# Performance work log

Measured on AMD Instinct MI355X. Metric: run time of the kernel, lower is better.

Reference implementation:

```python
import jax, jax.numpy as jnp
import numpy as np

D_MODEL = 1024
NUM_HEADS = 16
D_K = D_MODEL // NUM_HEADS  # 64


def setup_inputs() -> dict:
    key = jax.random.key(0)
    k1, k2, k3, k4, k5 = jax.random.split(key, 5)
    scale = 1.0 / np.sqrt(D_MODEL)
    x = jax.random.normal(k1, (2, 8192, D_MODEL), dtype=jnp.float32)
    W_qkv = jax.random.normal(k2, (D_MODEL, 3 * D_MODEL), dtype=jnp.float32) * scale
    b_qkv = jax.random.normal(k3, (3 * D_MODEL,), dtype=jnp.float32) * 0.01
    W_out = jax.random.normal(k4, (D_MODEL, D_MODEL), dtype=jnp.float32) * scale
    b_out = jax.random.normal(k5, (D_MODEL,), dtype=jnp.float32) * 0.01
    return {"x": x, "W_qkv": W_qkv, "b_qkv": b_qkv, "W_out": W_out, "b_out": b_out}


def reference(x, W_qkv, b_qkv, W_out, b_out):
    B, S, _ = x.shape
    # qkv: [B, S, 3*d_model] -> reshape [B, S, H, 3*d_k] (matches torch reshape:
    # head h owns contiguous slice [h*3dk:(h+1)*3dk], split into q/k/v of d_k each)
    qkv = (jnp.einsum('bsd,de->bse', x, W_qkv) + b_qkv).reshape(B, S, NUM_HEADS, 3 * D_K)
    q, k, v = qkv[..., :D_K], qkv[..., D_K:2 * D_K], qkv[..., 2 * D_K:]
    # NOTE: faithful to source — no head transpose, so matmul contracts d_k and
    # produces scores across the HEAD axis: [B, S, H, H]
    scores = jnp.einsum('bshd,bsgd->bshg', q, k) / np.sqrt(D_K)
    attn = jax.nn.softmax(scores, axis=-1)  # softmax over heads (g)
    context = jnp.einsum('bshg,bsgd->bshd', attn, v).reshape(B, S, NUM_HEADS * D_K)
    return jnp.einsum('bsd,de->bse', context, W_out) + b_out
```

## Files before the change

### kernel.cpp

```cpp
#include <hip/hip_runtime.h>
#include <hip/hip_bf16.h>

typedef short bf16x8 __attribute__((ext_vector_type(8)));
typedef float f32x4 __attribute__((ext_vector_type(4)));
typedef ushort ushort8_t __attribute__((ext_vector_type(8)));

__device__ __forceinline__ float bf2f(ushort u) {
    union { unsigned int i; float f; } c; c.i = ((unsigned int)u) << 16; return c.f;
}
__device__ __forceinline__ ushort f2bf(float f) {
    union { float f; unsigned int i; } c; c.f = f;
    unsigned int x = c.i;
    return (ushort)((x + 0x7fffu + ((x >> 16) & 1u)) >> 16);
}

#define GLOAD_LDS16(g, l) __builtin_amdgcn_global_load_lds( \
    (const __attribute__((address_space(1))) unsigned int*)(g), \
    (__attribute__((address_space(3))) unsigned int*)(l), 16, 0, 0)

__device__ __forceinline__ void transpose_cvt_body(const float* __restrict__ in,
                                                   ushort* __restrict__ out,
                                                   int K, int N, int bx, int by,
                                                   int tid, float (*tile)[33]) {
    int n0 = bx * 32, k0 = by * 32;
    int tx = tid & 31, ty = tid >> 5;
    #pragma unroll
    for (int i = 0; i < 32; i += 8)
        tile[ty + i][tx] = in[(size_t)(k0 + ty + i) * N + n0 + tx];
    __syncthreads();
    #pragma unroll
    for (int i = 0; i < 32; i += 8)
        out[(size_t)(n0 + ty + i) * K + k0 + tx] = f2bf(tile[tx][ty + i]);
}

__global__ __launch_bounds__(256) void k_prep(const float* __restrict__ x,
                                              ushort* __restrict__ xb,
                                              const float* __restrict__ Wq,
                                              ushort* __restrict__ wqkT,
                                              const float* __restrict__ Wo,
                                              ushort* __restrict__ woT) {
    __shared__ float tile[32][33];
    const int b = blockIdx.x, tid = threadIdx.x;
    if (b < 16384) {
        int i = b * 256 + tid;
        float4 v = ((const float4*)x)[i];
        ushort4 o;
        o.x = f2bf(v.x); o.y = f2bf(v.y); o.z = f2bf(v.z); o.w = f2bf(v.w);
        ((ushort4*)xb)[i] = o;
    } else if (b < 16384 + 3072) {
        int idx = b - 16384;
        transpose_cvt_body(Wq, wqkT, 1024, 3072, idx % 96, idx / 96, tid, tile);
    } else {
        int idx = b - (16384 + 3072);
        transpose_cvt_body(Wo, woT, 1024, 1024, idx & 31, idx >> 5, tid, tile);
    }
}


#define LDSA(c,kk) (lds + (c)*65536 + (kk)*16384)
#define LDSB(c,kk) (lds + (c)*65536 + 32768 + (kk)*16384)
#define STAGE_A(c,kk,col) do { \
    GLOAD_LDS16(gA0 + (col), LDSA(c,kk) + wave*1024); \
    GLOAD_LDS16(gA1 + (col), LDSA(c,kk) + 8192 + wave*1024); } while(0)
#define STAGE_B(c,kk,col) do { \
    GLOAD_LDS16(gB0 + (col), LDSB(c,kk) + wave*1024); \
    GLOAD_LDS16(gB1 + (col), LDSB(c,kk) + 8192 + wave*1024); } while(0)
#define READ_A8(c,kk) do { const char* _p = LDSA(c,kk) + aoff; \
    _Pragma("unroll") for (int m = 0; m < 8; ++m) af[m] = *(const bf16x8*)(_p + m*1024); } while(0)
#define READ_B2(c,kk,n0) do { const char* _p = LDSB(c,kk) + boff; \
    bfr[n0] = *(const bf16x8*)(_p + (n0)*1024); \
    bfr[(n0)+1] = *(const bf16x8*)(_p + ((n0)+1)*1024); } while(0)
#define MF16(n0) do { __builtin_amdgcn_s_setprio(1); \
    _Pragma("unroll") for (int m = 0; m < 8; ++m) { \
    acc[m][n0]     = __builtin_amdgcn_mfma_f32_16x16x32_bf16(af[m], bfr[n0],     acc[m][n0],     0,0,0); \
    acc[m][(n0)+1] = __builtin_amdgcn_mfma_f32_16x16x32_bf16(af[m], bfr[(n0)+1], acc[m][(n0)+1], 0,0,0); } \
    __builtin_amdgcn_s_setprio(0); } while(0)

#define BAR __builtin_amdgcn_s_barrier()
#define SB0 __builtin_amdgcn_sched_barrier(0)
#define VM10 asm volatile("s_waitcnt vmcnt(10)")
#define VM0  asm volatile("s_waitcnt vmcnt(0)")

#define PH1(reads, stage, mf, vm) do { reads; stage; mf; SB0; vm; BAR; SB0; } while(0)

#define ITERX(kb, LAST) do { \
   PH1( { READ_A8(0,0); READ_B2(0,0,0); }, STAGE_B(1,1,(kb)+96),              MF16(0), ); \
   PH1( { READ_B2(0,0,2); },               if(!(LAST)) STAGE_A(0,0,(kb)+128), MF16(2), if(LAST) VM0; else VM10 ); \
   PH1( { READ_A8(0,1); READ_B2(0,1,0); }, if(!(LAST)) STAGE_B(0,0,(kb)+128), MF16(0), ); \
   PH1( { READ_B2(0,1,2); },               if(!(LAST)) STAGE_A(0,1,(kb)+160), MF16(2), if(!(LAST)) VM10 ); \
   PH1( { READ_A8(1,0); READ_B2(1,0,0); }, if(!(LAST)) STAGE_B(0,1,(kb)+160), MF16(0), ); \
   PH1( { READ_B2(1,0,2); },               if(!(LAST)) STAGE_A(1,0,(kb)+192), MF16(2), if(!(LAST)) VM10 ); \
   PH1( { READ_A8(1,1); READ_B2(1,1,0); }, if(!(LAST)) STAGE_B(1,0,(kb)+192), MF16(0), ); \
   PH1( { READ_B2(1,1,2); },               if(!(LAST)) STAGE_A(1,1,(kb)+224), MF16(2), if(!(LAST)) VM10 ); \
} while(0)

template<bool OUT_BF16>
__global__ __launch_bounds__(512, 2) void k_gemm256(const ushort* __restrict__ A,
                                                    const ushort* __restrict__ Bt,
                                                    const float* __restrict__ bias,
                                                    void* __restrict__ Cout,
                                                    int N, int NTN) {
    __shared__ __align__(16) char lds[131072];
    const int K = 1024;
    const int tid = threadIdx.x;
    const int wave = tid >> 6, lane = tid & 63;
    const int wr = wave >> 2, wc = wave & 3;
    const int r = lane & 15, q = lane >> 4;

    const int cpx = gridDim.x >> 3, wg = blockIdx.x;
    const int swz = (wg & 7) * cpx + (wg >> 3);
    const int tm = swz / NTN, tn = swz - tm * NTN;
    const int bm = tm * 256, bn = tn * 256;

    const int srow = tid >> 2;
    const int c16l = (tid & 3) ^ ((srow >> 1) & 3);
    const ushort* gA0 = A  + (size_t)(bm + srow) * K + c16l * 8;
    const ushort* gA1 = gA0 + (size_t)128 * K;
    const ushort* gB0 = Bt + (size_t)(bn + srow) * K + c16l * 8;
    const ushort* gB1 = gB0 + (size_t)128 * K;

    const int chunkx = ((q ^ ((r >> 1) & 3)) << 4);
    const int aoff = (wr * 128 + r) * 64 + chunkx;
    const int boff = (wc * 64 + r) * 64 + chunkx;

    f32x4 acc[8][4];
    #pragma unroll
    for (int m = 0; m < 8; ++m)
        #pragma unroll
        for (int n = 0; n < 4; ++n)
            acc[m][n] = (f32x4){0.f, 0.f, 0.f, 0.f};
    bf16x8 af[8], bfr[4];

    STAGE_A(0,0,0);  STAGE_B(0,0,0);
    STAGE_A(0,1,32); STAGE_B(0,1,32);
    STAGE_A(1,0,64); STAGE_B(1,0,64);
    STAGE_A(1,1,96);
    VM10; BAR; SB0;

    #pragma unroll 1
    for (int i = 0; i < 7; ++i) { ITERX(i * 128, 0); }
    ITERX(896, 1);

    float* Cf = (float*)Cout;
    ushort* Cb = (ushort*)Cout;
    #pragma unroll
    for (int m = 0; m < 8; ++m) {
        int row0 = bm + wr * 128 + m * 16 + q * 4;
        #pragma unroll
        for (int n = 0; n < 4; ++n) {
            int col = bn + wc * 64 + n * 16 + r;
            float bv = bias[col];
            #pragma unroll
            for (int j = 0; j < 4; ++j) {
                float v = acc[m][n][j] + bv;
                if (OUT_BF16) Cb[(size_t)(row0 + j) * N + col] = f2bf(v);
                else          Cf[(size_t)(row0 + j) * N + col] = v;
            }
        }
    }
}

__global__ __launch_bounds__(256) void k_attn_mfma(const ushort* __restrict__ qkv,
                                                   ushort* __restrict__ ctx) {
    const int lane = threadIdx.x & 63;
    const size_t tok = (size_t)blockIdx.x * 4 + (threadIdx.x >> 6);
    const ushort* row = qkv + tok * 3072;
    const int r = lane & 15, g = lane >> 4;

    bf16x8 ka[2], qb[2];
    #pragma unroll
    for (int c = 0; c < 2; ++c) {
        ka[c] = *(const bf16x8*)(row + r * 192 + 64 + c * 32 + g * 8);
        qb[c] = *(const bf16x8*)(row + r * 192 +      c * 32 + g * 8);
    }
    f32x4 st = (f32x4){0.f, 0.f, 0.f, 0.f};
    st = __builtin_amdgcn_mfma_f32_16x16x32_bf16(ka[0], qb[0], st, 0, 0, 0);
    st = __builtin_amdgcn_mfma_f32_16x16x32_bf16(ka[1], qb[1], st, 0, 0, 0);

    float s[4];
    #pragma unroll
    for (int j = 0; j < 4; ++j) s[j] = st[j] * 0.125f;
    float m = fmaxf(fmaxf(s[0], s[1]), fmaxf(s[2], s[3]));
    m = fmaxf(m, __shfl_xor(m, 16));
    m = fmaxf(m, __shfl_xor(m, 32));
    float p[4], sum = 0.f;
    #pragma unroll
    for (int j = 0; j < 4; ++j) { p[j] = __expf(s[j] - m); sum += p[j]; }
    sum += __shfl_xor(sum, 16);
    sum += __shfl_xor(sum, 32);
    float inv = 1.f / sum;
    #pragma unroll
    for (int j = 0; j < 4; ++j) p[j] *= inv;

    const bool gok = (g < 2);
    const int src0 = (r + 32 * g) & 63, src1 = (src0 + 16) & 63;
    bf16x8 pa;
    #pragma unroll
    for (int j = 0; j < 4; ++j) {
        float a0 = __shfl(p[j], src0, 64);
        float a1 = __shfl(p[j], src1, 64);
        pa[j]     = (short)(gok ? f2bf(a0) : (ushort)0);
        pa[4 + j] = (short)(gok ? f2bf(a1) : (ushort)0);
    }

    #pragma unroll
    for (int db = 0; db < 4; ++db) {
        bf16x8 vb;
        #pragma unroll
        for (int j = 0; j < 8; ++j)
            vb[j] = (short)(gok ? row[(g * 8 + j) * 192 + 128 + db * 16 + r] : (ushort)0);
        f32x4 o = (f32x4){0.f, 0.f, 0.f, 0.f};
        o = __builtin_amdgcn_mfma_f32_16x16x32_bf16(pa, vb, o, 0, 0, 0);
        #pragma unroll
        for (int j = 0; j < 4; ++j)
            ctx[tok * 1024 + (4 * g + j) * 64 + db * 16 + r] = f2bf(o[j]);
    }
}

extern "C" void kernel_launch(void* const* d_in, const int* in_sizes, int n_in,
                              void* d_out, int out_size, void* d_ws, size_t ws_size,
                              hipStream_t stream) {
    const float* x     = (const float*)d_in[0];
    const float* W_qkv = (const float*)d_in[1];
    const float* b_qkv = (const float*)d_in[2];
    const float* W_out = (const float*)d_in[3];
    const float* b_out = (const float*)d_in[4];

    const int M = 16384, D = 1024, N3 = 3072;

    ushort* xb   = (ushort*)d_ws;
    ushort* wqkT = xb + (size_t)M * D;
    ushort* woT  = wqkT + (size_t)N3 * D;
    ushort* qkv  = woT + (size_t)D * D;
    ushort* ctx  = xb;

    hipLaunchKernelGGL(k_prep, dim3(16384 + 3072 + 1024), dim3(256), 0, stream,
                       x, xb, W_qkv, wqkT, W_out, woT);
    hipLaunchKernelGGL((k_gemm256<true>), dim3((N3 / 256) * (M / 256)), dim3(512), 0, stream,
                       xb, wqkT, b_qkv, (void*)qkv, N3, N3 / 256);
    hipLaunchKernelGGL(k_attn_mfma, dim3(M / 4), dim3(256), 0, stream, qkv, ctx);
    hipLaunchKernelGGL((k_gemm256<false>), dim3((D / 256) * (M / 256)), dim3(512), 0, stream,
                       ctx, woT, b_out, d_out, D, D / 256);
}
```

Measured before the change: 196.6 us.

## Switch GEMMs to 256x128 tiles with 4 waves and triple-buffered LDS

Replaces the 512-thread 256x256-tile GEMM with a 256-thread 256x128-tile kernel that uses a rotating three-stage LDS ring of 32-wide K slices instead of the two-buffer, two-substage schedule. Each workgroup uses about 72KB of LDS instead of 128KB, which allows more resident workgroups and doubles the grid size, improving wave coverage for the smaller output GEMM. In exchange, per-tile data reuse drops because B is shared across fewer rows, so global and LDS traffic per FLOP rises, and the loop now takes two barriers per 32-wide K step.

```diff
diff --git a/kernel.cpp b/kernel.cpp
--- a/kernel.cpp
+++ b/kernel.cpp
@@ -57,17 +57,19 @@
 }
 
 
-#define LDSA(c,kk) (lds + (c)*65536 + (kk)*16384)
-#define LDSB(c,kk) (lds + (c)*65536 + 32768 + (kk)*16384)
-#define STAGE_A(c,kk,col) do { \
-    GLOAD_LDS16(gA0 + (col), LDSA(c,kk) + wave*1024); \
-    GLOAD_LDS16(gA1 + (col), LDSA(c,kk) + 8192 + wave*1024); } while(0)
-#define STAGE_B(c,kk,col) do { \
-    GLOAD_LDS16(gB0 + (col), LDSB(c,kk) + wave*1024); \
-    GLOAD_LDS16(gB1 + (col), LDSB(c,kk) + 8192 + wave*1024); } while(0)
-#define READ_A8(c,kk) do { const char* _p = LDSA(c,kk) + aoff; \
+#define LDSA(c) (lds + (size_t)(c) * 24576)
+#define LDSB(c) (lds + (size_t)(c) * 24576 + 16384)
+#define STAGE_A(c,col) do { \
+    GLOAD_LDS16(gA0 + (col),                     LDSA(c) + wave*1024); \
+    GLOAD_LDS16(gA0 + (size_t) 64*1024 + (col),  LDSA(c) + 4096  + wave*1024); \
+    GLOAD_LDS16(gA0 + (size_t)128*1024 + (col),  LDSA(c) + 8192  + wave*1024); \
+    GLOAD_LDS16(gA0 + (size_t)192*1024 + (col),  LDSA(c) + 12288 + wave*1024); } while(0)
+#define STAGE_B(c,col) do { \
+    GLOAD_LDS16(gB0 + (col),                     LDSB(c) + wave*1024); \
+    GLOAD_LDS16(gB0 + (size_t) 64*1024 + (col),  LDSB(c) + 4096  + wave*1024); } while(0)
+#define READ_A8(c) do { const char* _p = LDSA(c) + aoff; \
     _Pragma("unroll") for (int m = 0; m < 8; ++m) af[m] = *(const bf16x8*)(_p + m*1024); } while(0)
-#define READ_B2(c,kk,n0) do { const char* _p = LDSB(c,kk) + boff; \
+#define READ_B2(c,n0) do { const char* _p = LDSB(c) + boff; \
     bfr[n0] = *(const bf16x8*)(_p + (n0)*1024); \
     bfr[(n0)+1] = *(const bf16x8*)(_p + ((n0)+1)*1024); } while(0)
 #define MF16(n0) do { __builtin_amdgcn_s_setprio(1); \
@@ -78,46 +80,31 @@
 
 #define BAR __builtin_amdgcn_s_barrier()
 #define SB0 __builtin_amdgcn_sched_barrier(0)
-#define VM10 asm volatile("s_waitcnt vmcnt(10)")
-#define VM0  asm volatile("s_waitcnt vmcnt(0)")
-
-#define PH1(reads, stage, mf, vm) do { reads; stage; mf; SB0; vm; BAR; SB0; } while(0)
-
-#define ITERX(kb, LAST) do { \
-   PH1( { READ_A8(0,0); READ_B2(0,0,0); }, STAGE_B(1,1,(kb)+96),              MF16(0), ); \
-   PH1( { READ_B2(0,0,2); },               if(!(LAST)) STAGE_A(0,0,(kb)+128), MF16(2), if(LAST) VM0; else VM10 ); \
-   PH1( { READ_A8(0,1); READ_B2(0,1,0); }, if(!(LAST)) STAGE_B(0,0,(kb)+128), MF16(0), ); \
-   PH1( { READ_B2(0,1,2); },               if(!(LAST)) STAGE_A(0,1,(kb)+160), MF16(2), if(!(LAST)) VM10 ); \
-   PH1( { READ_A8(1,0); READ_B2(1,0,0); }, if(!(LAST)) STAGE_B(0,1,(kb)+160), MF16(0), ); \
-   PH1( { READ_B2(1,0,2); },               if(!(LAST)) STAGE_A(1,0,(kb)+192), MF16(2), if(!(LAST)) VM10 ); \
-   PH1( { READ_A8(1,1); READ_B2(1,1,0); }, if(!(LAST)) STAGE_B(1,0,(kb)+192), MF16(0), ); \
-   PH1( { READ_B2(1,1,2); },               if(!(LAST)) STAGE_A(1,1,(kb)+224), MF16(2), if(!(LAST)) VM10 ); \
-} while(0)
+#define VM6 asm volatile("s_waitcnt vmcnt(6)")
+#define VM0 asm volatile("s_waitcnt vmcnt(0)")
 
 template<bool OUT_BF16>
-__global__ __launch_bounds__(512, 2) void k_gemm256(const ushort* __restrict__ A,
+__global__ __launch_bounds__(256, 2) void k_gemm128(const ushort* __restrict__ A,
                                                     const ushort* __restrict__ Bt,
                                                     const float* __restrict__ bias,
                                                     void* __restrict__ Cout,
                                                     int N, int NTN) {
-    __shared__ __align__(16) char lds[131072];
-    const int K = 1024;
+    __shared__ __align__(16) char lds[73728];
+    const int K = 1024, NT = 32;
     const int tid = threadIdx.x;
     const int wave = tid >> 6, lane = tid & 63;
-    const int wr = wave >> 2, wc = wave & 3;
+    const int wr = wave >> 1, wc = wave & 1;
     const int r = lane & 15, q = lane >> 4;
 
     const int cpx = gridDim.x >> 3, wg = blockIdx.x;
     const int swz = (wg & 7) * cpx + (wg >> 3);
     const int tm = swz / NTN, tn = swz - tm * NTN;
-    const int bm = tm * 256, bn = tn * 256;
+    const int bm = tm * 256, bn = tn * 128;
 
     const int srow = tid >> 2;
     const int c16l = (tid & 3) ^ ((srow >> 1) & 3);
     const ushort* gA0 = A  + (size_t)(bm + srow) * K + c16l * 8;
-    const ushort* gA1 = gA0 + (size_t)128 * K;
     const ushort* gB0 = Bt + (size_t)(bn + srow) * K + c16l * 8;
-    const ushort* gB1 = gB0 + (size_t)128 * K;
 
     const int chunkx = ((q ^ ((r >> 1) & 3)) << 4);
     const int aoff = (wr * 128 + r) * 64 + chunkx;
@@ -131,15 +118,25 @@
             acc[m][n] = (f32x4){0.f, 0.f, 0.f, 0.f};
     bf16x8 af[8], bfr[4];
 
-    STAGE_A(0,0,0);  STAGE_B(0,0,0);
-    STAGE_A(0,1,32); STAGE_B(0,1,32);
-    STAGE_A(1,0,64); STAGE_B(1,0,64);
-    STAGE_A(1,1,96);
-    VM10; BAR; SB0;
-
+    STAGE_A(0, 0);  STAGE_B(0, 0);
+    STAGE_A(1, 32); STAGE_B(1, 32);
+    VM6; BAR; SB0;
+
+    int ca = 0, cb = 1, cs = 2;
     #pragma unroll 1
-    for (int i = 0; i < 7; ++i) { ITERX(i * 128, 0); }
-    ITERX(896, 1);
+    for (int t = 0; t < NT; ++t) {
+        READ_A8(ca); READ_B2(ca, 0);
+        if (t < NT - 2) STAGE_A(cs, (t + 2) * 32);
+        MF16(0);
+        SB0; BAR; SB0;
+        READ_B2(ca, 2);
+        if (t < NT - 2) STAGE_B(cs, (t + 2) * 32);
+        MF16(2);
+        SB0;
+        if (t < NT - 2) VM6; else if (t == NT - 2) VM0;
+        BAR; SB0;
+        int tmp = ca; ca = cb; cb = cs; cs = tmp;
+    }
 
     float* Cf = (float*)Cout;
     ushort* Cb = (ushort*)Cout;
@@ -236,9 +233,9 @@
 
     hipLaunchKernelGGL(k_prep, dim3(16384 + 3072 + 1024), dim3(256), 0, stream,
                        x, xb, W_qkv, wqkT, W_out, woT);
-    hipLaunchKernelGGL((k_gemm256<true>), dim3((N3 / 256) * (M / 256)), dim3(512), 0, stream,
-                       xb, wqkT, b_qkv, (void*)qkv, N3, N3 / 256);
+    hipLaunchKernelGGL((k_gemm128<true>), dim3((N3 / 128) * (M / 256)), dim3(256), 0, stream,
+                       xb, wqkT, b_qkv, (void*)qkv, N3, N3 / 128);
     hipLaunchKernelGGL(k_attn_mfma, dim3(M / 4), dim3(256), 0, stream, qkv, ctx);
-    hipLaunchKernelGGL((k_gemm256<false>), dim3((D / 256) * (M / 256)), dim3(512), 0, stream,
-                       ctx, woT, b_out, d_out, D, D / 256);
-}
+    hipLaunchKernelGGL((k_gemm128<false>), dim3((D / 128) * (M / 256)), dim3(256), 0, stream,
+                       ctx, woT, b_out, d_out, D, D / 128);
+}
```

Result: slower. 201.8 us (+2.6%).
